# Optimization experiments

Measured on AMD Instinct MI355X. Metric: run time of the kernel, lower is better.

## Reference

```python
import jax, jax.numpy as jnp
import numpy as np

B, S, H, D, R = 16, 2048, 1024, 64, 2048  # batch, seq_len, hidden, inner_dim, num_relations


def setup_inputs() -> dict:
    key = jax.random.key(0)
    k1, k2, k3, k4 = jax.random.split(key, 4)
    last_hidden_state = jax.random.normal(k1, (B, S, H), dtype=jnp.float32)
    W = jax.random.normal(k2, (H, 2 * D), dtype=jnp.float32) * (H ** -0.5)
    b = jnp.zeros((2 * D,), dtype=jnp.float32)
    position_ids = jnp.tile(jnp.arange(S, dtype=jnp.int32), (B, 1))
    relations_idx = jax.random.randint(k3, (B, R, 4), 0, S, dtype=jnp.int32)
    labels_mask = (jax.random.uniform(k4, (B, R)) > 0.1).astype(jnp.float32)
    return {
        'last_hidden_state': last_hidden_state,
        'W': W,
        'b': b,
        'position_ids': position_ids,
        'relations_idx': relations_idx,
        'labels_mask': labels_mask,
    }


def reference(last_hidden_state, W, b, position_ids, relations_idx, labels_mask):
    # linear projection -> split into q/k halves
    outputs = last_hidden_state @ W + b            # [B,S,2D]
    qw, kw = outputs[..., :D], outputs[..., D:]    # each [B,S,D]

    # RoPE (interleaved sin/cos layout matching torch stack+reshape)
    inv_freq = jnp.power(10000.0, -2.0 * jnp.arange(D // 2, dtype=jnp.float32) / D)
    ang = position_ids[..., None].astype(jnp.float32) * inv_freq  # [B,S,D/2]
    sin_pos = jnp.repeat(jnp.sin(ang), 2, axis=-1)  # [B,S,D]
    cos_pos = jnp.repeat(jnp.cos(ang), 2, axis=-1)  # [B,S,D]

    def rotate(x):
        x2 = jnp.stack([-x[..., 1::2], x[..., ::2]], axis=-1).reshape(x.shape)
        return x * cos_pos + x2 * sin_pos

    qw = rotate(qw)
    kw = rotate(kw)

    # gather span endpoints: relations_idx[...,k] -> [B,R], take along seq axis
    def gather(x, idx):
        return jnp.take_along_axis(x, idx[..., None], axis=1)  # [B,R,D]

    sub_qw = jnp.concatenate([gather(qw, relations_idx[:, :, 0]),
                              gather(qw, relations_idx[:, :, 1])], axis=-1)  # [B,R,2D]
    obj_kw = jnp.concatenate([gather(kw, relations_idx[:, :, 2]),
                              gather(kw, relations_idx[:, :, 3])], axis=-1)  # [B,R,2D]

    logits = jnp.sum(sub_qw * obj_kw, axis=-1)     # [B,R]
    logits = logits + (1.0 - labels_mask) * -1e12
    return logits / jnp.sqrt(jnp.float32(D))
```

## Files before the change

### kernel.cpp

```cpp
#include <hip/hip_runtime.h>
#include <hip/hip_bf16.h>
#include <cstdint>

#define B_ 16
#define S_ 2048
#define H_ 1024
#define D_ 64
#define R_ 2048
#define M_ (B_*S_)
#define N_ 128
#define NC_ 16

typedef short short8 __attribute__((ext_vector_type(8)));
typedef float f32x4  __attribute__((ext_vector_type(4)));

__device__ __forceinline__ unsigned short f2bf(float f) {
    unsigned u = __builtin_bit_cast(unsigned, f);
    u += 0x7FFFu + ((u >> 16) & 1u);
    return (unsigned short)(u >> 16);
}
__device__ __forceinline__ unsigned pk2(float a, float b) {
    return (unsigned)f2bf(a) | ((unsigned)f2bf(b) << 16);
}
__device__ __forceinline__ unsigned pkt(float a, float b) {
    return (__builtin_bit_cast(unsigned, a) >> 16) |
           (__builtin_bit_cast(unsigned, b) & 0xFFFF0000u);
}
__device__ __forceinline__ float bflo(unsigned u) {
    return __builtin_bit_cast(float, u << 16);
}
__device__ __forceinline__ float bfhi(unsigned u) {
    return __builtin_bit_cast(float, u & 0xFFFF0000u);
}

typedef const __attribute__((address_space(1))) void gvoid_t;
typedef __attribute__((address_space(3))) void lvoid_t;
__device__ __forceinline__ void gload16(const void* g, void* l) {
    __builtin_amdgcn_global_load_lds((gvoid_t*)g, (lvoid_t*)l, 16, 0, 0);
}

__global__ void build_wt(const float* __restrict__ W, unsigned short* __restrict__ Wt) {
    __shared__ unsigned short lt[N_ * 34];
    const int t  = threadIdx.x;
    const int bk = blockIdx.x;
    const int kr = t >> 7, cn = t & 127;
    #pragma unroll
    for (int i = 0; i < 16; i++) {
        const int k = i * 2 + kr;
        lt[cn * 34 + k] = f2bf(W[(size_t)(bk * 32 + k) * N_ + cn]);
    }
    __syncthreads();
    const int kk = t & 31, nr = t >> 5;
    #pragma unroll
    for (int i = 0; i < 16; i++) {
        const int n = i * 8 + nr;
        Wt[(size_t)n * H_ + bk * 32 + kk] = lt[n * 34 + kk];
    }
}

__launch_bounds__(256, 3)
__global__ void gemm_rope(const float* __restrict__ A,
                          const unsigned short* __restrict__ Wt,
                          const float* __restrict__ bias,
                          const int* __restrict__ pos_ids,
                          unsigned* __restrict__ qk)
{
    __shared__ __align__(16) float          abuf[2][32 * 64];
    __shared__ __align__(16) unsigned short wbuf[2][N_ * 64];

    const int tid   = threadIdx.x;
    const int wavei = tid >> 6, lane = tid & 63;
    const int ln15  = lane & 15, quad = lane >> 4;
    const int rg    = wavei >> 1, ch = wavei & 1;
    const int m0    = blockIdx.x * 32;

    const float* a_src[2]; int a_dst[2];
    #pragma unroll
    for (int c = 0; c < 2; c++) {
        const int u = c * 256 + tid;
        const int row = u >> 4, i = u & 15;
        a_src[c] = A + (size_t)(m0 + row) * H_ + ((i ^ (row & 7)) << 2);
        a_dst[c] = u << 2;
    }
    const unsigned short* w_src[4]; int w_dst[4];
    #pragma unroll
    for (int t = 0; t < 4; t++) {
        const int u = t * 256 + tid;
        const int n = u >> 3, i = u & 7;
        w_src[t] = Wt + (size_t)n * H_ + ((i ^ (n & 7)) << 3);
        w_dst[t] = u << 3;
    }

    f32x4 acc[4];
    #pragma unroll
    for (int j = 0; j < 4; j++) acc[j] = (f32x4)0.f;

    #pragma unroll
    for (int c = 0; c < 2; c++) gload16(a_src[c], &abuf[0][a_dst[c]]);
    #pragma unroll
    for (int t = 0; t < 4; t++) gload16(w_src[t], &wbuf[0][w_dst[t]]);

    const int arow = rg * 16 + ln15;
    const int key  = ln15 & 7;

    for (int kc = 0; kc < NC_; kc++) {
        __syncthreads();
        if (kc + 1 < NC_) {
            const int nb = (kc + 1) & 1;
            #pragma unroll
            for (int c = 0; c < 2; c++)
                gload16(a_src[c] + (kc + 1) * 64, &abuf[nb][a_dst[c]]);
            #pragma unroll
            for (int t = 0; t < 4; t++)
                gload16(w_src[t] + (kc + 1) * 64, &wbuf[nb][w_dst[t]]);
        }
        const int cb = kc & 1;
        const float* ab = &abuf[cb][arow * 64];
        #pragma unroll
        for (int ks = 0; ks < 2; ks++) {
            const int g0 = ks * 8 + quad * 2;
            const f32x4 r0 = *(const f32x4*)(ab + ((g0 ^ key) << 2));
            const f32x4 r1 = *(const f32x4*)(ab + (((g0 + 1) ^ key) << 2));
            int4 ai;
            ai.x = (int)pkt(r0[0], r0[1]);
            ai.y = (int)pkt(r0[2], r0[3]);
            ai.z = (int)pkt(r1[0], r1[1]);
            ai.w = (int)pkt(r1[2], r1[3]);
            const short8 af = __builtin_bit_cast(short8, ai);
            const int p = (((ks * 4 + quad) ^ key) << 3);
            #pragma unroll
            for (int j = 0; j < 4; j++) {
                const int n = ch * 64 + j * 16 + ln15;
                const short8 bf = *(const short8*)(&wbuf[cb][n * 64 + p]);
                acc[j] = __builtin_amdgcn_mfma_f32_16x16x32_bf16(af, bf, acc[j], 0, 0, 0);
            }
        }
    }

    const int nb = ch * 64;
    float bv[4], invr[4];
    #pragma unroll
    for (int j = 0; j < 4; j++) bv[j] = bias[nb + j * 16 + ln15];
    #pragma unroll
    for (int j = 0; j < 4; j++) {
        const float fi = (float)((j * 16 + ln15) >> 1);
        invr[j] = exp2f(fi * -0.41524101186092029f) * 0.15915494309189535f;
    }
    const bool odd = (ln15 & 1);
    const int rbase = m0 + rg * 16 + quad * 4;
    #pragma unroll
    for (int reg = 0; reg < 4; reg++) {
        const int row = rbase + reg;
        const float pos = (float)pos_ids[row];
        #pragma unroll
        for (int j = 0; j < 4; j++) {
            float v = acc[j][reg] + bv[j];
            float p = __shfl_xor(v, 1, 64);
            float fr = __builtin_amdgcn_fractf(pos * invr[j]);
            float s  = __builtin_amdgcn_sinf(fr);
            float co = __builtin_amdgcn_cosf(fr);
            float outv = odd ? fmaf(v, co, p * s) : fmaf(v, co, -p * s);
            float po = __shfl_xor(outv, 1, 64);
            if (!odd)
                qk[(size_t)row * 64 + ch * 32 + j * 8 + (ln15 >> 1)] = pk2(outv, po);
        }
    }
}

__global__ void gather_dot(const unsigned* __restrict__ qk, const int* __restrict__ rel,
                           const float* __restrict__ mask, float* __restrict__ out)
{
    const int w    = (blockIdx.x * 256 + threadIdx.x) >> 6;
    const int lane = threadIdx.x & 63;
    const int b    = w >> 11;
    const int4 id4 = ((const int4*)rel)[w];
    const unsigned* base = qk + (size_t)b * S_ * 64;
    const int rq  = (lane < 32) ? id4.x : id4.y;
    const int rk  = (lane < 32) ? id4.z : id4.w;
    const int col = lane & 31;
    const unsigned uq = base[(size_t)rq * 64 + col];
    const unsigned uk = base[(size_t)rk * 64 + 32 + col];
    float v = bflo(uq) * bflo(uk) + bfhi(uq) * bfhi(uk);
    #pragma unroll
    for (int off = 32; off; off >>= 1) v += __shfl_xor(v, off, 64);
    if (lane == 0)
        out[w] = (v + (1.0f - mask[w]) * -1e12f) * 0.125f;
}

extern "C" void kernel_launch(void* const* d_in, const int* in_sizes, int n_in,
                              void* d_out, int out_size, void* d_ws, size_t ws_size,
                              hipStream_t stream) {
    const float* lhs  = (const float*)d_in[0];
    const float* W    = (const float*)d_in[1];
    const float* bias = (const float*)d_in[2];
    const int*   pos  = (const int*)d_in[3];
    const int*   rel  = (const int*)d_in[4];
    const float* mask = (const float*)d_in[5];
    float* out = (float*)d_out;

    unsigned short* Wt = (unsigned short*)d_ws;
    unsigned* qk = (unsigned*)((char*)d_ws + (size_t)N_ * H_ * 2);

    build_wt<<<32, 256, 0, stream>>>(W, Wt);
    gemm_rope<<<1024, 256, 0, stream>>>(lhs, Wt, bias, pos, qk);
    gather_dot<<<8192, 256, 0, stream>>>(qk, rel, mask, out);
}
```

Before: 232.1 us.

## Enlarge GEMM row tile and prefetch A/W through registers with bf16 LDS staging

The projection GEMM now handles 64 rows per block instead of 32, so each wave computes two 16-row tiles and every W fragment read from LDS is used twice. Direct global-to-LDS loads are replaced by register prefetch two chunks ahead. A is converted to bf16 before it is written to LDS, which halves A's shared-memory footprint and removes the per-MFMA conversion from the inner loop. This halves the grid to 512 blocks and raises register pressure, which may reduce the number of resident waves available to hide memory latency.

```diff
diff --git a/kernel.cpp b/kernel.cpp
--- a/kernel.cpp
+++ b/kernel.cpp
@@ -33,12 +33,6 @@
     return __builtin_bit_cast(float, u & 0xFFFF0000u);
 }
 
-typedef const __attribute__((address_space(1))) void gvoid_t;
-typedef __attribute__((address_space(3))) void lvoid_t;
-__device__ __forceinline__ void gload16(const void* g, void* l) {
-    __builtin_amdgcn_global_load_lds((gvoid_t*)g, (lvoid_t*)l, 16, 0, 0);
-}
-
 __global__ void build_wt(const float* __restrict__ W, unsigned short* __restrict__ Wt) {
     __shared__ unsigned short lt[N_ * 34];
     const int t  = threadIdx.x;
@@ -65,79 +59,113 @@
                           const int* __restrict__ pos_ids,
                           unsigned* __restrict__ qk)
 {
-    __shared__ __align__(16) float          abuf[2][32 * 64];
+    __shared__ __align__(16) unsigned short abuf[2][64 * 64];
     __shared__ __align__(16) unsigned short wbuf[2][N_ * 64];
 
     const int tid   = threadIdx.x;
     const int wavei = tid >> 6, lane = tid & 63;
     const int ln15  = lane & 15, quad = lane >> 4;
-    const int rg    = wavei >> 1, ch = wavei & 1;
-    const int m0    = blockIdx.x * 32;
+    const int rw    = wavei >> 1, cw = wavei & 1;
+    const int m0    = blockIdx.x * 64;
 
     const float* a_src[2]; int a_dst[2];
     #pragma unroll
-    for (int c = 0; c < 2; c++) {
-        const int u = c * 256 + tid;
-        const int row = u >> 4, i = u & 15;
-        a_src[c] = A + (size_t)(m0 + row) * H_ + ((i ^ (row & 7)) << 2);
-        a_dst[c] = u << 2;
+    for (int t = 0; t < 2; t++) {
+        const int u = t * 256 + tid;
+        const int r = u >> 3, oc = u & 7;
+        a_src[t] = A + (size_t)(m0 + r) * H_ + oc * 8;
+        a_dst[t] = r * 64 + ((oc ^ (r & 7)) * 8);
     }
     const unsigned short* w_src[4]; int w_dst[4];
     #pragma unroll
     for (int t = 0; t < 4; t++) {
         const int u = t * 256 + tid;
-        const int n = u >> 3, i = u & 7;
-        w_src[t] = Wt + (size_t)n * H_ + ((i ^ (n & 7)) << 3);
-        w_dst[t] = u << 3;
-    }
-
-    f32x4 acc[4];
-    #pragma unroll
-    for (int j = 0; j < 4; j++) acc[j] = (f32x4)0.f;
-
-    #pragma unroll
-    for (int c = 0; c < 2; c++) gload16(a_src[c], &abuf[0][a_dst[c]]);
-    #pragma unroll
-    for (int t = 0; t < 4; t++) gload16(w_src[t], &wbuf[0][w_dst[t]]);
-
-    const int arow = rg * 16 + ln15;
-    const int key  = ln15 & 7;
+        const int n = u >> 3, oc = u & 7;
+        w_src[t] = Wt + (size_t)n * H_ + oc * 8;
+        w_dst[t] = n * 64 + ((oc ^ (n & 7)) * 8);
+    }
+
+    f32x4  ra[2][2];
+    short8 rwv[4];
+
+    f32x4 acc[8];
+    #pragma unroll
+    for (int i = 0; i < 8; i++) acc[i] = (f32x4)0.f;
+
+    #pragma unroll
+    for (int t = 0; t < 2; t++) {
+        ra[t][0] = *(const f32x4*)(a_src[t]);
+        ra[t][1] = *(const f32x4*)(a_src[t] + 4);
+    }
+    #pragma unroll
+    for (int t = 0; t < 4; t++) rwv[t] = *(const short8*)(w_src[t]);
+    #pragma unroll
+    for (int t = 0; t < 2; t++) {
+        int4 p;
+        p.x = (int)pkt(ra[t][0][0], ra[t][0][1]);
+        p.y = (int)pkt(ra[t][0][2], ra[t][0][3]);
+        p.z = (int)pkt(ra[t][1][0], ra[t][1][1]);
+        p.w = (int)pkt(ra[t][1][2], ra[t][1][3]);
+        *(short8*)(&abuf[0][a_dst[t]]) = __builtin_bit_cast(short8, p);
+    }
+    #pragma unroll
+    for (int t = 0; t < 4; t++) *(short8*)(&wbuf[0][w_dst[t]]) = rwv[t];
+    #pragma unroll
+    for (int t = 0; t < 2; t++) {
+        ra[t][0] = *(const f32x4*)(a_src[t] + 64);
+        ra[t][1] = *(const f32x4*)(a_src[t] + 68);
+    }
+    #pragma unroll
+    for (int t = 0; t < 4; t++) rwv[t] = *(const short8*)(w_src[t] + 64);
+
+    const int key = ln15 & 7;
 
     for (int kc = 0; kc < NC_; kc++) {
         __syncthreads();
         if (kc + 1 < NC_) {
             const int nb = (kc + 1) & 1;
             #pragma unroll
-            for (int c = 0; c < 2; c++)
-                gload16(a_src[c] + (kc + 1) * 64, &abuf[nb][a_dst[c]]);
-            #pragma unroll
-            for (int t = 0; t < 4; t++)
-                gload16(w_src[t] + (kc + 1) * 64, &wbuf[nb][w_dst[t]]);
+            for (int t = 0; t < 2; t++) {
+                int4 p;
+                p.x = (int)pkt(ra[t][0][0], ra[t][0][1]);
+                p.y = (int)pkt(ra[t][0][2], ra[t][0][3]);
+                p.z = (int)pkt(ra[t][1][0], ra[t][1][1]);
+                p.w = (int)pkt(ra[t][1][2], ra[t][1][3]);
+                *(short8*)(&abuf[nb][a_dst[t]]) = __builtin_bit_cast(short8, p);
+            }
+            #pragma unroll
+            for (int t = 0; t < 4; t++) *(short8*)(&wbuf[nb][w_dst[t]]) = rwv[t];
+        }
+        if (kc + 2 < NC_) {
+            const int o = (kc + 2) * 64;
+            #pragma unroll
+            for (int t = 0; t < 2; t++) {
+                ra[t][0] = *(const f32x4*)(a_src[t] + o);
+                ra[t][1] = *(const f32x4*)(a_src[t] + o + 4);
+            }
+            #pragma unroll
+            for (int t = 0; t < 4; t++) rwv[t] = *(const short8*)(w_src[t] + o);
         }
         const int cb = kc & 1;
-        const float* ab = &abuf[cb][arow * 64];
         #pragma unroll
         for (int ks = 0; ks < 2; ks++) {
-            const int g0 = ks * 8 + quad * 2;
-            const f32x4 r0 = *(const f32x4*)(ab + ((g0 ^ key) << 2));
-            const f32x4 r1 = *(const f32x4*)(ab + (((g0 + 1) ^ key) << 2));
-            int4 ai;
-            ai.x = (int)pkt(r0[0], r0[1]);
-            ai.y = (int)pkt(r0[2], r0[3]);
-            ai.z = (int)pkt(r1[0], r1[1]);
-            ai.w = (int)pkt(r1[2], r1[3]);
-            const short8 af = __builtin_bit_cast(short8, ai);
-            const int p = (((ks * 4 + quad) ^ key) << 3);
+            const int oc = ((ks * 4 + quad) ^ key) * 8;
+            short8 af[2];
+            #pragma unroll
+            for (int rt = 0; rt < 2; rt++)
+                af[rt] = *(const short8*)(&abuf[cb][(rw * 32 + rt * 16 + ln15) * 64 + oc]);
             #pragma unroll
             for (int j = 0; j < 4; j++) {
-                const int n = ch * 64 + j * 16 + ln15;
-                const short8 bf = *(const short8*)(&wbuf[cb][n * 64 + p]);
-                acc[j] = __builtin_amdgcn_mfma_f32_16x16x32_bf16(af, bf, acc[j], 0, 0, 0);
-            }
-        }
-    }
-
-    const int nb = ch * 64;
+                const short8 bf = *(const short8*)(&wbuf[cb][(cw * 64 + j * 16 + ln15) * 64 + oc]);
+                #pragma unroll
+                for (int rt = 0; rt < 2; rt++)
+                    acc[rt * 4 + j] = __builtin_amdgcn_mfma_f32_16x16x32_bf16(
+                                          af[rt], bf, acc[rt * 4 + j], 0, 0, 0);
+            }
+        }
+    }
+
+    const int nb = cw * 64;
     float bv[4], invr[4];
     #pragma unroll
     for (int j = 0; j < 4; j++) bv[j] = bias[nb + j * 16 + ln15];
@@ -147,22 +175,25 @@
         invr[j] = exp2f(fi * -0.41524101186092029f) * 0.15915494309189535f;
     }
     const bool odd = (ln15 & 1);
-    const int rbase = m0 + rg * 16 + quad * 4;
-    #pragma unroll
-    for (int reg = 0; reg < 4; reg++) {
-        const int row = rbase + reg;
-        const float pos = (float)pos_ids[row];
+    #pragma unroll
+    for (int rt = 0; rt < 2; rt++) {
+        const int rbase = m0 + rw * 32 + rt * 16 + quad * 4;
         #pragma unroll
-        for (int j = 0; j < 4; j++) {
-            float v = acc[j][reg] + bv[j];
-            float p = __shfl_xor(v, 1, 64);
-            float fr = __builtin_amdgcn_fractf(pos * invr[j]);
-            float s  = __builtin_amdgcn_sinf(fr);
-            float co = __builtin_amdgcn_cosf(fr);
-            float outv = odd ? fmaf(v, co, p * s) : fmaf(v, co, -p * s);
-            float po = __shfl_xor(outv, 1, 64);
-            if (!odd)
-                qk[(size_t)row * 64 + ch * 32 + j * 8 + (ln15 >> 1)] = pk2(outv, po);
+        for (int reg = 0; reg < 4; reg++) {
+            const int row = rbase + reg;
+            const float pos = (float)pos_ids[row];
+            #pragma unroll
+            for (int j = 0; j < 4; j++) {
+                float v = acc[rt * 4 + j][reg] + bv[j];
+                float p = __shfl_xor(v, 1, 64);
+                float fr = __builtin_amdgcn_fractf(pos * invr[j]);
+                float s  = __builtin_amdgcn_sinf(fr);
+                float co = __builtin_amdgcn_cosf(fr);
+                float outv = odd ? fmaf(v, co, p * s) : fmaf(v, co, -p * s);
+                float po = __shfl_xor(outv, 1, 64);
+                if (!odd)
+                    qk[(size_t)row * 64 + cw * 32 + j * 8 + (ln15 >> 1)] = pk2(outv, po);
+            }
         }
     }
 }
@@ -202,6 +233,6 @@
     unsigned* qk = (unsigned*)((char*)d_ws + (size_t)N_ * H_ * 2);
 
     build_wt<<<32, 256, 0, stream>>>(W, Wt);
-    gemm_rope<<<1024, 256, 0, stream>>>(lhs, Wt, bias, pos, qk);
+    gemm_rope<<<512, 256, 0, stream>>>(lhs, Wt, bias, pos, qk);
     gather_dot<<<8192, 256, 0, stream>>>(qk, rel, mask, out);
 }
```

After: 224.1 us. 1.04x faster.

## Load A directly into registers and stage W via registers with 2-wave blocks

Applied to the files above, without the earlier changes.

The GEMM kernel stops staging the fp32 activation tile through LDS with async global_load_lds. Each lane instead reads its own A fragment straight into registers, prefetched two k-chunks ahead. W tiles are loaded into registers and then written to swizzled LDS. Blocks shrink from 4 to 2 waves, and each wave now computes all 128 output columns for its 16 rows. This removes the LDS traffic for A and the duplicated A reads across column halves, at the cost of higher register pressure and lower occupancy per block.

```diff
diff --git a/kernel.cpp b/kernel.cpp
--- a/kernel.cpp
+++ b/kernel.cpp
@@ -33,12 +33,6 @@
     return __builtin_bit_cast(float, u & 0xFFFF0000u);
 }
 
-typedef const __attribute__((address_space(1))) void gvoid_t;
-typedef __attribute__((address_space(3))) void lvoid_t;
-__device__ __forceinline__ void gload16(const void* g, void* l) {
-    __builtin_amdgcn_global_load_lds((gvoid_t*)g, (lvoid_t*)l, 16, 0, 0);
-}
-
 __global__ void build_wt(const float* __restrict__ W, unsigned short* __restrict__ Wt) {
     __shared__ unsigned short lt[N_ * 34];
     const int t  = threadIdx.x;
@@ -58,111 +52,120 @@
     }
 }
 
-__launch_bounds__(256, 3)
+__launch_bounds__(128, 2)
 __global__ void gemm_rope(const float* __restrict__ A,
                           const unsigned short* __restrict__ Wt,
                           const float* __restrict__ bias,
                           const int* __restrict__ pos_ids,
                           unsigned* __restrict__ qk)
 {
-    __shared__ __align__(16) float          abuf[2][32 * 64];
     __shared__ __align__(16) unsigned short wbuf[2][N_ * 64];
 
-    const int tid   = threadIdx.x;
-    const int wavei = tid >> 6, lane = tid & 63;
-    const int ln15  = lane & 15, quad = lane >> 4;
-    const int rg    = wavei >> 1, ch = wavei & 1;
-    const int m0    = blockIdx.x * 32;
-
-    const float* a_src[2]; int a_dst[2];
-    #pragma unroll
-    for (int c = 0; c < 2; c++) {
-        const int u = c * 256 + tid;
-        const int row = u >> 4, i = u & 15;
-        a_src[c] = A + (size_t)(m0 + row) * H_ + ((i ^ (row & 7)) << 2);
-        a_dst[c] = u << 2;
-    }
-    const unsigned short* w_src[4]; int w_dst[4];
-    #pragma unroll
-    for (int t = 0; t < 4; t++) {
-        const int u = t * 256 + tid;
-        const int n = u >> 3, i = u & 7;
-        w_src[t] = Wt + (size_t)n * H_ + ((i ^ (n & 7)) << 3);
-        w_dst[t] = u << 3;
-    }
-
-    f32x4 acc[4];
-    #pragma unroll
-    for (int j = 0; j < 4; j++) acc[j] = (f32x4)0.f;
-
-    #pragma unroll
-    for (int c = 0; c < 2; c++) gload16(a_src[c], &abuf[0][a_dst[c]]);
-    #pragma unroll
-    for (int t = 0; t < 4; t++) gload16(w_src[t], &wbuf[0][w_dst[t]]);
-
-    const int arow = rg * 16 + ln15;
-    const int key  = ln15 & 7;
-
+    const int tid  = threadIdx.x;
+    const int wv   = tid >> 6, lane = tid & 63;
+    const int ln15 = lane & 15, quad = lane >> 4, key = ln15 & 7;
+    const int m0   = blockIdx.x * 32;
+    const int row  = m0 + wv * 16 + ln15;
+
+    const float* a_base = A + (size_t)row * H_ + quad * 8;
+
+    const unsigned short* w_src[8]; int w_dst[8];
+    #pragma unroll
+    for (int i = 0; i < 8; i++) {
+        const int u = i * 128 + tid;
+        const int n = u >> 3, oc = u & 7;
+        w_src[i] = Wt + (size_t)n * H_ + oc * 8;
+        w_dst[i] = n * 64 + ((oc ^ (n & 7)) * 8);
+    }
+
+    f32x4  areg[2][4];
+    short8 wreg[2][8];
+    f32x4  acc[8];
+    #pragma unroll
+    for (int j = 0; j < 8; j++) acc[j] = (f32x4)0.f;
+
+    #pragma unroll
+    for (int ks = 0; ks < 2; ks++)
+        #pragma unroll
+        for (int h = 0; h < 2; h++) {
+            areg[0][ks * 2 + h] = *(const f32x4*)(a_base + ks * 32 + h * 4);
+            areg[1][ks * 2 + h] = *(const f32x4*)(a_base + 64 + ks * 32 + h * 4);
+        }
+    #pragma unroll
+    for (int i = 0; i < 8; i++) wreg[0][i] = *(const short8*)(w_src[i]);
+    #pragma unroll
+    for (int i = 0; i < 8; i++) *(short8*)(&wbuf[0][w_dst[i]]) = wreg[0][i];
+    #pragma unroll
+    for (int i = 0; i < 8; i++) wreg[1][i] = *(const short8*)(w_src[i] + 64);
+
+    #pragma unroll
     for (int kc = 0; kc < NC_; kc++) {
+        const int cb = kc & 1, nb = cb ^ 1;
         __syncthreads();
         if (kc + 1 < NC_) {
-            const int nb = (kc + 1) & 1;
-            #pragma unroll
-            for (int c = 0; c < 2; c++)
-                gload16(a_src[c] + (kc + 1) * 64, &abuf[nb][a_dst[c]]);
-            #pragma unroll
-            for (int t = 0; t < 4; t++)
-                gload16(w_src[t] + (kc + 1) * 64, &wbuf[nb][w_dst[t]]);
-        }
-        const int cb = kc & 1;
-        const float* ab = &abuf[cb][arow * 64];
+            #pragma unroll
+            for (int i = 0; i < 8; i++)
+                *(short8*)(&wbuf[nb][w_dst[i]]) = wreg[nb][i];
+        }
+        short8 af[2];
         #pragma unroll
         for (int ks = 0; ks < 2; ks++) {
-            const int g0 = ks * 8 + quad * 2;
-            const f32x4 r0 = *(const f32x4*)(ab + ((g0 ^ key) << 2));
-            const f32x4 r1 = *(const f32x4*)(ab + (((g0 + 1) ^ key) << 2));
-            int4 ai;
-            ai.x = (int)pkt(r0[0], r0[1]);
-            ai.y = (int)pkt(r0[2], r0[3]);
-            ai.z = (int)pkt(r1[0], r1[1]);
-            ai.w = (int)pkt(r1[2], r1[3]);
-            const short8 af = __builtin_bit_cast(short8, ai);
-            const int p = (((ks * 4 + quad) ^ key) << 3);
-            #pragma unroll
-            for (int j = 0; j < 4; j++) {
-                const int n = ch * 64 + j * 16 + ln15;
-                const short8 bf = *(const short8*)(&wbuf[cb][n * 64 + p]);
-                acc[j] = __builtin_amdgcn_mfma_f32_16x16x32_bf16(af, bf, acc[j], 0, 0, 0);
+            const f32x4 r0 = areg[cb][ks * 2 + 0];
+            const f32x4 r1 = areg[cb][ks * 2 + 1];
+            int4 p;
+            p.x = (int)pkt(r0[0], r0[1]);
+            p.y = (int)pkt(r0[2], r0[3]);
+            p.z = (int)pkt(r1[0], r1[1]);
+            p.w = (int)pkt(r1[2], r1[3]);
+            af[ks] = __builtin_bit_cast(short8, p);
+        }
+        if (kc + 2 < NC_) {
+            const int o = (kc + 2) * 64;
+            #pragma unroll
+            for (int ks = 0; ks < 2; ks++)
+                #pragma unroll
+                for (int h = 0; h < 2; h++)
+                    areg[cb][ks * 2 + h] = *(const f32x4*)(a_base + o + ks * 32 + h * 4);
+            #pragma unroll
+            for (int i = 0; i < 8; i++)
+                wreg[cb][i] = *(const short8*)(w_src[i] + o);
+        }
+        #pragma unroll
+        for (int ks = 0; ks < 2; ks++) {
+            const int g = ((ks * 4 + quad) ^ key) * 8;
+            #pragma unroll
+            for (int j = 0; j < 8; j++) {
+                const short8 bf = *(const short8*)(&wbuf[cb][(j * 16 + ln15) * 64 + g]);
+                acc[j] = __builtin_amdgcn_mfma_f32_16x16x32_bf16(af[ks], bf, acc[j], 0, 0, 0);
             }
         }
     }
 
-    const int nb = ch * 64;
-    float bv[4], invr[4];
-    #pragma unroll
-    for (int j = 0; j < 4; j++) bv[j] = bias[nb + j * 16 + ln15];
+    float bv[8], invr[4];
+    #pragma unroll
+    for (int j = 0; j < 8; j++) bv[j] = bias[j * 16 + ln15];
     #pragma unroll
     for (int j = 0; j < 4; j++) {
         const float fi = (float)((j * 16 + ln15) >> 1);
         invr[j] = exp2f(fi * -0.41524101186092029f) * 0.15915494309189535f;
     }
     const bool odd = (ln15 & 1);
-    const int rbase = m0 + rg * 16 + quad * 4;
+    const int rbase = m0 + wv * 16 + quad * 4;
     #pragma unroll
     for (int reg = 0; reg < 4; reg++) {
-        const int row = rbase + reg;
-        const float pos = (float)pos_ids[row];
-        #pragma unroll
-        for (int j = 0; j < 4; j++) {
+        const int r = rbase + reg;
+        const float pos = (float)pos_ids[r];
+        #pragma unroll
+        for (int j = 0; j < 8; j++) {
             float v = acc[j][reg] + bv[j];
             float p = __shfl_xor(v, 1, 64);
-            float fr = __builtin_amdgcn_fractf(pos * invr[j]);
+            float fr = __builtin_amdgcn_fractf(pos * invr[j & 3]);
             float s  = __builtin_amdgcn_sinf(fr);
             float co = __builtin_amdgcn_cosf(fr);
             float outv = odd ? fmaf(v, co, p * s) : fmaf(v, co, -p * s);
             float po = __shfl_xor(outv, 1, 64);
             if (!odd)
-                qk[(size_t)row * 64 + ch * 32 + j * 8 + (ln15 >> 1)] = pk2(outv, po);
+                qk[(size_t)r * 64 + j * 8 + (ln15 >> 1)] = pk2(outv, po);
         }
     }
 }
@@ -202,6 +205,6 @@
     unsigned* qk = (unsigned*)((char*)d_ws + (size_t)N_ * H_ * 2);
 
     build_wt<<<32, 256, 0, stream>>>(W, Wt);
-    gemm_rope<<<1024, 256, 0, stream>>>(lhs, Wt, bias, pos, qk);
+    gemm_rope<<<1024, 128, 0, stream>>>(lhs, Wt, bias, pos, qk);
     gather_dot<<<8192, 256, 0, stream>>>(qk, rel, mask, out);
 }
```

After: 225.1 us. 3.0% less time.
